# Kernel optimization log

Hardware: AMD Instinct MI355X
Metric: run time of the kernel (lower is better)

The kernel has to match this reference:

```python
import jax, jax.numpy as jnp
import numpy as np

TAU = 0.07
MIN_PIXELS = 3
LAMBDA_CF = 0.5
NUM_INST = 16  # labels in patch_mask are 0 (bg) .. NUM_INST
N, D = 65536, 256


def _l2norm(x, axis=-1):
    n = jnp.linalg.norm(x, axis=axis, keepdims=True)
    return x / jnp.maximum(n, 1e-12)


def setup_inputs() -> dict:
    key = jax.random.key(0)
    k1, k2, k3 = jax.random.split(key, 3)
    dp = jax.random.normal(k1, (N, D), dtype=jnp.float32)
    f_cf = jax.random.normal(k2, (N, D), dtype=jnp.float32)
    patch_mask = jax.random.randint(k3, (N,), 0, NUM_INST + 1, dtype=jnp.int32)
    return {"dp": dp, "f_cf": f_cf, "patch_mask": patch_mask}


def reference(dp, f_cf, patch_mask):
    K1 = NUM_INST + 1  # segment 0 = background, 1..K = instances
    labels = patch_mask
    dpn = _l2norm(dp)       # [N, D]
    cfn = _l2norm(f_cf)     # [N, D]

    ones = jnp.ones((labels.shape[0],), dtype=dp.dtype)
    cnt = jax.ops.segment_sum(ones, labels, num_segments=K1)         # [K1]
    sum_dp = jax.ops.segment_sum(dpn, labels, num_segments=K1)       # [K1, D]
    sum_cf = jax.ops.segment_sum(cfn, labels, num_segments=K1)       # [K1, D]
    safe_cnt = jnp.maximum(cnt, 1.0)

    mu_dp = _l2norm(sum_dp / safe_cnt[:, None])   # per-segment normalized mean of dp
    mu_cf = _l2norm(sum_cf / safe_cnt[:, None])   # per-segment normalized mean of f_cf
    mu_bg_dp = mu_dp[0]                           # [D]
    mu_bg_cf = mu_cf[0]                           # [D]

    # per-pixel similarities
    pos_t = jnp.sum(dpn * mu_dp[labels], axis=-1)      # dp . mu_{k(label)}
    neg_t = dpn @ mu_bg_dp                             # dp . mu_bg
    # -log(exp(p/tau)/(exp(p/tau)+exp(n/tau))) == softplus((n-p)/tau)
    pix_loss_t = jax.nn.softplus((neg_t - pos_t) / TAU)

    pos_cf = cfn @ mu_bg_cf                            # f_cf . mu_bg_cf (the 'pos' in the cf term)
    oth_cf = jnp.sum(cfn * mu_cf[labels], axis=-1)     # f_cf . mu_k_cf
    pix_loss_cf = jax.nn.softplus((oth_cf - pos_cf) / TAU)

    seg_loss_t = jax.ops.segment_sum(pix_loss_t, labels, num_segments=K1) / safe_cnt
    seg_loss_cf = jax.ops.segment_sum(pix_loss_cf, labels, num_segments=K1) / safe_cnt

    inst_ids = jnp.arange(K1)
    valid = (inst_ids > 0) & (cnt >= MIN_PIXELS)       # instances with enough pixels
    n_valid = jnp.maximum(jnp.sum(valid.astype(dp.dtype)), 1.0)

    loss_t = jnp.sum(jnp.where(valid, seg_loss_t, 0.0)) / n_valid
    loss_cf = jnp.sum(jnp.where(valid, seg_loss_cf, 0.0)) / n_valid
    return loss_t + LAMBDA_CF * loss_cf
```

## Files before the change

kernel.cpp:

```cpp
#include <hip/hip_runtime.h>
#include <math.h>

#define K1 17
#define SEG_F (K1 * 256)
#define PART_F (2 * SEG_F + 32)
#define NGRP 8
#define NPART 256

#define SCALE_SUM 65536.0f
#define INV_SUM   (1.0f / 65536.0f)
#define SCALE_L   8192.0f
#define INV_L     (1.0f / 8192.0f)
#define FP8_SCALE 16.0f
#define TAU_INV   (1.0f / 0.07f)

#define GRED_BASE 0
#define MU_BASE   (NGRP * 2 * SEG_F)
#define GCNT_OFF  (MU_BASE + 2 * SEG_F)
#define LT_OFF    (GCNT_OFF + K1)
#define LC_OFF    (LT_OFF + K1)
#define PART_BASE 78400
#define FP8D_BASE (PART_BASE + NPART * PART_F)

typedef float v2f __attribute__((ext_vector_type(2)));

template <int CTRL, int RMASK>
__device__ __forceinline__ float dpp_add(float x) {
    int t = __builtin_amdgcn_update_dpp(0, __float_as_int(x), CTRL, RMASK, 0xf, false);
    return x + __int_as_float(t);
}
__device__ __forceinline__ float wave_sum_nb(float x) {
    x = dpp_add<0x111, 0xf>(x);
    x = dpp_add<0x112, 0xf>(x);
    x = dpp_add<0x114, 0xf>(x);
    x = dpp_add<0x118, 0xf>(x);
    x = dpp_add<0x142, 0xa>(x);
    x = dpp_add<0x143, 0xc>(x);
    return x;
}
__device__ __forceinline__ float wave_sum(float x) {
    return __int_as_float(__builtin_amdgcn_readlane(__float_as_int(wave_sum_nb(x)), 63));
}
__device__ __forceinline__ float dot4s(const float4 v) {
    return v.x * v.x + v.y * v.y + v.z * v.z + v.w * v.w;
}
__device__ __forceinline__ float softplus_f(float x) {
    const float a = -fabsf(x) * 1.4426950408889634f;
    float e; asm("v_exp_f32 %0, %1" : "=v"(e) : "v"(a));
    float l; asm("v_log_f32 %0, %1" : "=v"(l) : "v"(1.0f + e));
    return fmaxf(x, 0.0f) + l * 0.6931471805599453f;
}
__device__ __forceinline__ float rsq_f(float x) {
    float r; asm("v_rsq_f32 %0, %1" : "=v"(r) : "v"(x));
    return r;
}

template <bool W8>
__device__ __forceinline__ void kA_commit(int* __restrict__ s, const float4 v, const float4 w,
                                          float nd, float nc, int l, int lane,
                                          uint2* __restrict__ q8)
{
    const float ir = rsq_f(fmaxf(nd, 1e-24f));
    const float jr = rsq_f(fmaxf(nc, 1e-24f));
    const float f = SCALE_SUM * ir;
    const float g = SCALE_SUM * jr;
    int* a = s + l * 256 + lane;
    atomicAdd(a,       (int)(v.x * f));
    atomicAdd(a + 64,  (int)(v.y * f));
    atomicAdd(a + 128, (int)(v.z * f));
    atomicAdd(a + 192, (int)(v.w * f));
    int* b = a + SEG_F;
    atomicAdd(b,       (int)(w.x * g));
    atomicAdd(b + 64,  (int)(w.y * g));
    atomicAdd(b + 128, (int)(w.z * g));
    atomicAdd(b + 192, (int)(w.w * g));
    if (W8) {
        const float fe = FP8_SCALE * ir;
        const float ge = FP8_SCALE * jr;
        int pd = __builtin_amdgcn_cvt_pk_fp8_f32(v.x * fe, v.y * fe, 0, false);
        pd     = __builtin_amdgcn_cvt_pk_fp8_f32(v.z * fe, v.w * fe, pd, true);
        int pc = __builtin_amdgcn_cvt_pk_fp8_f32(w.x * ge, w.y * ge, 0, false);
        pc     = __builtin_amdgcn_cvt_pk_fp8_f32(w.z * ge, w.w * ge, pc, true);
        *q8 = make_uint2((unsigned)pd, (unsigned)pc);
    }
}

template <bool W8>
__global__ __launch_bounds__(1024) void kA(const float4* __restrict__ dp, const float4* __restrict__ cf,
                                           const int* __restrict__ mask, float* __restrict__ part,
                                           uint2* __restrict__ q, int nPart, int nRows)
{
    __shared__ int s[2 * SEG_F];
    __shared__ int hist[K1];
    const int tid = threadIdx.x;
    for (int i = tid; i < 2 * SEG_F; i += 1024) s[i] = 0;
    if (tid < K1) hist[tid] = 0;
    __syncthreads();

    const int lane = tid & 63;
    const int wid = tid >> 6;
    const int rpb = (nRows + nPart - 1) / nPart;
    const int base = blockIdx.x * rpb;
    const int end = (base + rpb < nRows) ? base + rpb : nRows;

    int r = base + wid;
    for (; r + 16 < end; r += 32) {
        const int l0 = mask[r], l1 = mask[r + 16];
        const float4 v0 = dp[(size_t)r * 64 + lane];
        const float4 w0 = cf[(size_t)r * 64 + lane];
        const float4 v1 = dp[(size_t)(r + 16) * 64 + lane];
        const float4 w1 = cf[(size_t)(r + 16) * 64 + lane];
        const float nd0 = wave_sum(dot4s(v0));
        const float nc0 = wave_sum(dot4s(w0));
        const float nd1 = wave_sum(dot4s(v1));
        const float nc1 = wave_sum(dot4s(w1));
        kA_commit<W8>(s, v0, w0, nd0, nc0, l0, lane, q + (size_t)r * 64 + lane);
        kA_commit<W8>(s, v1, w1, nd1, nc1, l1, lane, q + (size_t)(r + 16) * 64 + lane);
        if (lane == 0) { atomicAdd(&hist[l0], 1); atomicAdd(&hist[l1], 1); }
    }
    for (; r < end; r += 16) {
        const int l0 = mask[r];
        const float4 v0 = dp[(size_t)r * 64 + lane];
        const float4 w0 = cf[(size_t)r * 64 + lane];
        const float nd0 = wave_sum(dot4s(v0));
        const float nc0 = wave_sum(dot4s(w0));
        kA_commit<W8>(s, v0, w0, nd0, nc0, l0, lane, q + (size_t)r * 64 + lane);
        if (lane == 0) atomicAdd(&hist[l0], 1);
    }
    __syncthreads();
    float* outp = part + (size_t)blockIdx.x * PART_F;
    for (int i = tid; i < 2 * SEG_F; i += 1024) outp[i] = (float)s[i] * INV_SUM;
    if (tid < K1) outp[2 * SEG_F + tid] = (float)hist[tid];
}

__global__ __launch_bounds__(256) void kRed(const float* __restrict__ part, float* __restrict__ gred, int nPart)
{
    const int col = blockIdx.x * 256 + threadIdx.x;
    const int g = blockIdx.y;
    const int per = nPart / NGRP;
    const float* p = part + (size_t)g * per * PART_F + col;
    float acc = 0.0f;
    for (int b = 0; b < per; ++b) acc += p[(size_t)b * PART_F];
    gred[g * (2 * SEG_F) + col] = acc;
}

__global__ __launch_bounds__(256) void k_mu(float* __restrict__ ws, int nPart)
{
    const int k = blockIdx.x, t = threadIdx.x;
    if (k == 0 && t < 2 * K1) ((int*)ws)[LT_OFF + t] = 0;
    __shared__ float C[256];
    float c = 0.0f;
    for (int b = t; b < nPart; b += 256) c += ws[PART_BASE + (size_t)b * PART_F + 2 * SEG_F + k];
    C[t] = c; __syncthreads();
    for (int s2 = 128; s2 > 0; s2 >>= 1) { if (t < s2) C[t] += C[t + s2]; __syncthreads(); }
    const float cnt = C[0];
    __syncthreads();
    float c0 = 0.0f;
    for (int b = t; b < nPart; b += 256) c0 += ws[PART_BASE + (size_t)b * PART_F + 2 * SEG_F];
    C[t] = c0; __syncthreads();
    for (int s2 = 128; s2 > 0; s2 >>= 1) { if (t < s2) C[t] += C[t + s2]; __syncthreads(); }
    const float cnt0 = C[0];

    const float safek = fmaxf(cnt, 1.0f), safe0 = fmaxf(cnt0, 1.0f);
    float sdk = 0, sck = 0, sd0 = 0, sc0 = 0;
    #pragma unroll
    for (int g = 0; g < NGRP; ++g) {
        const float* gr = ws + GRED_BASE + g * 2 * SEG_F;
        sdk += gr[k * 256 + t];  sck += gr[SEG_F + k * 256 + t];
        sd0 += gr[t];            sc0 += gr[SEG_F + t];
    }
    const float mdk = sdk / safek, mck = sck / safek;
    const float md0 = sd0 / safe0, mc0 = sc0 / safe0;
    __shared__ float A[256], B[256];
    A[t] = mdk * mdk; B[t] = mck * mck;
    __syncthreads();
    for (int s2 = 128; s2 > 0; s2 >>= 1) { if (t < s2) { A[t] += A[t + s2]; B[t] += B[t + s2]; } __syncthreads(); }
    const float idk = 1.0f / fmaxf(sqrtf(A[0]), 1e-12f);
    const float ick = 1.0f / fmaxf(sqrtf(B[0]), 1e-12f);
    __syncthreads();
    A[t] = md0 * md0; B[t] = mc0 * mc0;
    __syncthreads();
    for (int s2 = 128; s2 > 0; s2 >>= 1) { if (t < s2) { A[t] += A[t + s2]; B[t] += B[t + s2]; } __syncthreads(); }
    const float id0 = 1.0f / fmaxf(sqrtf(A[0]), 1e-12f);
    const float ic0 = 1.0f / fmaxf(sqrtf(B[0]), 1e-12f);
    const int dnat = 4 * (t & 63) + (t >> 6);
    ws[MU_BASE + k * 256 + dnat]         = md0 * id0 - mdk * idk;
    ws[MU_BASE + SEG_F + k * 256 + dnat] = mck * ick - mc0 * ic0;
    if (t == 0) ws[GCNT_OFF + k] = cnt;
}

__device__ __forceinline__ void q_commit(float dd, float dc, int l, int isl63,
                                         int* __restrict__ lt, int* __restrict__ lc)
{
    const float xt = dd * (TAU_INV / FP8_SCALE);
    const float xc = dc * (TAU_INV / FP8_SCALE);
    const float plt = softplus_f(xt);
    const float plc = softplus_f(xc);
    if (isl63) {
        atomicAdd(&lt[l], (int)(plt * SCALE_L + 0.5f));
        atomicAdd(&lc[l], (int)(plc * SCALE_L + 0.5f));
    }
}
__global__ __launch_bounds__(512) void k_loss8(const uint2* __restrict__ q,
                                               const int* __restrict__ mask, float* __restrict__ ws,
                                               int nBlocks, int nRows)
{
    __shared__ float4 dmud[SEG_F / 4], dmuc[SEG_F / 4];
    __shared__ int lt[K1], lc[K1];
    const int tid = threadIdx.x;
    const float4* musrc = (const float4*)(ws + MU_BASE);
    for (int i = tid; i < SEG_F / 4; i += 512) { dmud[i] = musrc[i]; dmuc[i] = musrc[SEG_F / 4 + i]; }
    if (tid < K1) { lt[tid] = 0; lc[tid] = 0; }
    __syncthreads();

    const int lane = tid & 63;
    const int wid = tid >> 6;
    const int rpb = (nRows + nBlocks - 1) / nBlocks;
    const int base = blockIdx.x * rpb;
    const int end = (base + rpb < nRows) ? base + rpb : nRows;
    const int isl63 = (lane == 63);

    int r = base + wid;
    for (; r + 8 < end; r += 16) {
        const int l0 = mask[r], l1 = mask[r + 8];
        const uint2 q0 = q[(size_t)r * 64 + lane];
        const uint2 q1 = q[(size_t)(r + 8) * 64 + lane];
        const float4 D0 = dmud[l0 * 64 + lane], C0 = dmuc[l0 * 64 + lane];
        const float4 D1 = dmud[l1 * 64 + lane], C1 = dmuc[l1 * 64 + lane];
        const v2f al0 = __builtin_amdgcn_cvt_pk_f32_fp8((int)q0.x, false), ah0 = __builtin_amdgcn_cvt_pk_f32_fp8((int)q0.x, true);
        const v2f bl0 = __builtin_amdgcn_cvt_pk_f32_fp8((int)q0.y, false), bh0 = __builtin_amdgcn_cvt_pk_f32_fp8((int)q0.y, true);
        const v2f al1 = __builtin_amdgcn_cvt_pk_f32_fp8((int)q1.x, false), ah1 = __builtin_amdgcn_cvt_pk_f32_fp8((int)q1.x, true);
        const v2f bl1 = __builtin_amdgcn_cvt_pk_f32_fp8((int)q1.y, false), bh1 = __builtin_amdgcn_cvt_pk_f32_fp8((int)q1.y, true);
        float dd0 = al0.x * D0.x + al0.y * D0.y + ah0.x * D0.z + ah0.y * D0.w;
        float dc0 = bl0.x * C0.x + bl0.y * C0.y + bh0.x * C0.z + bh0.y * C0.w;
        float dd1 = al1.x * D1.x + al1.y * D1.y + ah1.x * D1.z + ah1.y * D1.w;
        float dc1 = bl1.x * C1.x + bl1.y * C1.y + bh1.x * C1.z + bh1.y * C1.w;
        dd0 = wave_sum_nb(dd0); dc0 = wave_sum_nb(dc0);
        dd1 = wave_sum_nb(dd1); dc1 = wave_sum_nb(dc1);
        q_commit(dd0, dc0, l0, isl63, lt, lc);
        q_commit(dd1, dc1, l1, isl63, lt, lc);
    }
    for (; r < end; r += 8) {
        const int l0 = mask[r];
        const uint2 q0 = q[(size_t)r * 64 + lane];
        const float4 D0 = dmud[l0 * 64 + lane], C0 = dmuc[l0 * 64 + lane];
        const v2f al0 = __builtin_amdgcn_cvt_pk_f32_fp8((int)q0.x, false), ah0 = __builtin_amdgcn_cvt_pk_f32_fp8((int)q0.x, true);
        const v2f bl0 = __builtin_amdgcn_cvt_pk_f32_fp8((int)q0.y, false), bh0 = __builtin_amdgcn_cvt_pk_f32_fp8((int)q0.y, true);
        float dd0 = al0.x * D0.x + al0.y * D0.y + ah0.x * D0.z + ah0.y * D0.w;
        float dc0 = bl0.x * C0.x + bl0.y * C0.y + bh0.x * C0.z + bh0.y * C0.w;
        dd0 = wave_sum_nb(dd0); dc0 = wave_sum_nb(dc0);
        q_commit(dd0, dc0, l0, isl63, lt, lc);
    }
    __syncthreads();
    if (tid < K1) {
        atomicAdd((int*)ws + LT_OFF + tid, lt[tid]);
        atomicAdd((int*)ws + LC_OFF + tid, lc[tid]);
    }
}

__global__ __launch_bounds__(512) void k_lossraw(const float4* __restrict__ dp, const float4* __restrict__ cf,
                                                 const int* __restrict__ mask, float* __restrict__ ws,
                                                 int nBlocks, int nRows)
{
    __shared__ float4 dmud[SEG_F / 4], dmuc[SEG_F / 4];
    __shared__ int lt[K1], lc[K1];
    const int tid = threadIdx.x;
    const float4* musrc = (const float4*)(ws + MU_BASE);
    for (int i = tid; i < SEG_F / 4; i += 512) { dmud[i] = musrc[i]; dmuc[i] = musrc[SEG_F / 4 + i]; }
    if (tid < K1) { lt[tid] = 0; lc[tid] = 0; }
    __syncthreads();

    const int lane = tid & 63;
    const int wid = tid >> 6;
    const int rpb = (nRows + nBlocks - 1) / nBlocks;
    const int base = blockIdx.x * rpb;
    const int end = (base + rpb < nRows) ? base + rpb : nRows;
    const int isl63 = (lane == 63);

    for (int r = base + wid; r < end; r += 8) {
        const int l0 = mask[r];
        const float4 v0 = dp[(size_t)r * 64 + lane];
        const float4 w0 = cf[(size_t)r * 64 + lane];
        const float4 D0 = dmud[l0 * 64 + lane], C0 = dmuc[l0 * 64 + lane];
        float nd = dot4s(v0), nc = dot4s(w0);
        float dd = v0.x * D0.x + v0.y * D0.y + v0.z * D0.z + v0.w * D0.w;
        float dc = w0.x * C0.x + w0.y * C0.y + w0.z * C0.z + w0.w * C0.w;
        nd = wave_sum_nb(nd); nc = wave_sum_nb(nc);
        dd = wave_sum_nb(dd); dc = wave_sum_nb(dc);
        const float xt = dd * rsq_f(fmaxf(nd, 1e-24f)) * TAU_INV;
        const float xc = dc * rsq_f(fmaxf(nc, 1e-24f)) * TAU_INV;
        const float plt = softplus_f(xt);
        const float plc = softplus_f(xc);
        if (isl63) {
            atomicAdd(&lt[l0], (int)(plt * SCALE_L + 0.5f));
            atomicAdd(&lc[l0], (int)(plc * SCALE_L + 0.5f));
        }
    }
    __syncthreads();
    if (tid < K1) {
        atomicAdd((int*)ws + LT_OFF + tid, lt[tid]);
        atomicAdd((int*)ws + LC_OFF + tid, lc[tid]);
    }
}

__global__ void k_final(const float* __restrict__ ws, float* __restrict__ out)
{
    const int t = threadIdx.x;
    const int* LT = (const int*)ws + LT_OFF;
    const int* LC = (const int*)ws + LC_OFF;
    float vt = 0.0f, vc = 0.0f, nv = 0.0f;
    if (t >= 1 && t < K1) {
        const float cnt = ws[GCNT_OFF + t];
        if (cnt >= 3.0f) {
            const float safe = fmaxf(cnt, 1.0f);
            vt = (float)LT[t] * INV_L / safe;
            vc = (float)LC[t] * INV_L / safe;
            nv = 1.0f;
        }
    }
    #pragma unroll
    for (int o = 32; o > 0; o >>= 1) {
        vt += __shfl_xor(vt, o, 64);
        vc += __shfl_xor(vc, o, 64);
        nv += __shfl_xor(nv, o, 64);
    }
    if (t == 0) {
        const float n = fmaxf(nv, 1.0f);
        out[0] = vt / n + 0.5f * (vc / n);
    }
}

extern "C" void kernel_launch(void* const* d_in, const int* in_sizes, int n_in,
                              void* d_out, int out_size, void* d_ws, size_t ws_size,
                              hipStream_t stream)
{
    const float4* dp = (const float4*)d_in[0];
    const float4* cf = (const float4*)d_in[1];
    const int* mask  = (const int*)d_in[2];
    float* ws  = (float*)d_ws;
    float* out = (float*)d_out;
    const int nRows = in_sizes[2];

    uint2* q = (uint2*)((unsigned*)ws + FP8D_BASE);
    const bool use8 = (ws_size / 4) >= (size_t)FP8D_BASE + 2 * (size_t)nRows * 64;

    if (use8)
        kA<true><<<NPART, 1024, 0, stream>>>(dp, cf, mask, ws + PART_BASE, q, NPART, nRows);
    else
        kA<false><<<NPART, 1024, 0, stream>>>(dp, cf, mask, ws + PART_BASE, q, NPART, nRows);
    kRed<<<dim3(34, NGRP), 256, 0, stream>>>(ws + PART_BASE, ws + GRED_BASE, NPART);
    k_mu<<<K1, 256, 0, stream>>>(ws, NPART);
    const int nB3 = 1024;
    if (use8)
        k_loss8<<<nB3, 512, 0, stream>>>(q, mask, ws, nB3, nRows);
    else
        k_lossraw<<<nB3, 512, 0, stream>>>(dp, cf, mask, ws, nB3, nRows);
    k_final<<<1, 64, 0, stream>>>(ws, out);
}
```

Baseline: 80.60 us.

## Unroll kA to four rows per wave and fold final reduction into loss kernel

The first kernel now loads four dp/cf row pairs per wave per iteration instead of two, with asm keep-alive hints so the loads are issued together before the reductions. This raises memory-level parallelism in the bandwidth-bound normalisation pass at the cost of more registers. Separately, the standalone k_final launch is removed. Its work moves into a last-block-done epilogue of the loss kernel, driven by an atomic counter that k_mu zeroes, which saves one kernel launch and its gap.

Result: no change. 81.64 us (+1.3%).

```diff
diff --git a/kernel.cpp b/kernel.cpp
--- a/kernel.cpp
+++ b/kernel.cpp
@@ -19,10 +19,13 @@
 #define GCNT_OFF  (MU_BASE + 2 * SEG_F)
 #define LT_OFF    (GCNT_OFF + K1)
 #define LC_OFF    (LT_OFF + K1)
+#define DONE_OFF  (LC_OFF + K1)
 #define PART_BASE 78400
 #define FP8D_BASE (PART_BASE + NPART * PART_F)
 
 typedef float v2f __attribute__((ext_vector_type(2)));
+
+#define KEEP4(v) asm volatile("" :: "v"((v).x), "v"((v).y), "v"((v).z), "v"((v).w))
 
 template <int CTRL, int RMASK>
 __device__ __forceinline__ float dpp_add(float x) {
@@ -104,19 +107,30 @@
     const int end = (base + rpb < nRows) ? base + rpb : nRows;
 
     int r = base + wid;
-    for (; r + 16 < end; r += 32) {
-        const int l0 = mask[r], l1 = mask[r + 16];
-        const float4 v0 = dp[(size_t)r * 64 + lane];
-        const float4 w0 = cf[(size_t)r * 64 + lane];
-        const float4 v1 = dp[(size_t)(r + 16) * 64 + lane];
-        const float4 w1 = cf[(size_t)(r + 16) * 64 + lane];
-        const float nd0 = wave_sum(dot4s(v0));
-        const float nc0 = wave_sum(dot4s(w0));
-        const float nd1 = wave_sum(dot4s(v1));
-        const float nc1 = wave_sum(dot4s(w1));
+    for (; r + 48 < end; r += 64) {
+        const int l0 = mask[r], l1 = mask[r + 16], l2 = mask[r + 32], l3 = mask[r + 48];
+        float4 v0 = dp[(size_t)r * 64 + lane],        w0 = cf[(size_t)r * 64 + lane];
+        float4 v1 = dp[(size_t)(r + 16) * 64 + lane], w1 = cf[(size_t)(r + 16) * 64 + lane];
+        float4 v2 = dp[(size_t)(r + 32) * 64 + lane], w2 = cf[(size_t)(r + 32) * 64 + lane];
+        float4 v3 = dp[(size_t)(r + 48) * 64 + lane], w3 = cf[(size_t)(r + 48) * 64 + lane];
+        KEEP4(v0); KEEP4(w0); KEEP4(v1); KEEP4(w1);
+        KEEP4(v2); KEEP4(w2); KEEP4(v3); KEEP4(w3);
+        float nd0 = dot4s(v0), nc0 = dot4s(w0);
+        float nd1 = dot4s(v1), nc1 = dot4s(w1);
+        float nd2 = dot4s(v2), nc2 = dot4s(w2);
+        float nd3 = dot4s(v3), nc3 = dot4s(w3);
+        nd0 = wave_sum(nd0); nc0 = wave_sum(nc0);
+        nd1 = wave_sum(nd1); nc1 = wave_sum(nc1);
+        nd2 = wave_sum(nd2); nc2 = wave_sum(nc2);
+        nd3 = wave_sum(nd3); nc3 = wave_sum(nc3);
         kA_commit<W8>(s, v0, w0, nd0, nc0, l0, lane, q + (size_t)r * 64 + lane);
         kA_commit<W8>(s, v1, w1, nd1, nc1, l1, lane, q + (size_t)(r + 16) * 64 + lane);
-        if (lane == 0) { atomicAdd(&hist[l0], 1); atomicAdd(&hist[l1], 1); }
+        kA_commit<W8>(s, v2, w2, nd2, nc2, l2, lane, q + (size_t)(r + 32) * 64 + lane);
+        kA_commit<W8>(s, v3, w3, nd3, nc3, l3, lane, q + (size_t)(r + 48) * 64 + lane);
+        if (lane == 0) {
+            atomicAdd(&hist[l0], 1); atomicAdd(&hist[l1], 1);
+            atomicAdd(&hist[l2], 1); atomicAdd(&hist[l3], 1);
+        }
     }
     for (; r < end; r += 16) {
         const int l0 = mask[r];
@@ -147,7 +161,7 @@
 __global__ __launch_bounds__(256) void k_mu(float* __restrict__ ws, int nPart)
 {
     const int k = blockIdx.x, t = threadIdx.x;
-    if (k == 0 && t < 2 * K1) ((int*)ws)[LT_OFF + t] = 0;
+    if (k == 0 && t < 2 * K1 + 1) ((int*)ws)[LT_OFF + t] = 0;
     __shared__ float C[256];
     float c = 0.0f;
     for (int b = t; b < nPart; b += 256) c += ws[PART_BASE + (size_t)b * PART_F + 2 * SEG_F + k];
@@ -189,6 +203,45 @@
     if (t == 0) ws[GCNT_OFF + k] = cnt;
 }
 
+__device__ __forceinline__ void loss_epilogue(float* __restrict__ ws, float* __restrict__ out,
+                                              int* __restrict__ lt, int* __restrict__ lc,
+                                              int tid, int nBlocks)
+{
+    __syncthreads();
+    int* LT = (int*)ws + LT_OFF;
+    int* LC = (int*)ws + LC_OFF;
+    if (tid < K1) {
+        atomicAdd(&LT[tid], lt[tid]);
+        atomicAdd(&LC[tid], lc[tid]);
+    }
+    __syncthreads();
+    __shared__ int amLast;
+    if (tid == 0) amLast = (atomicAdd((int*)ws + DONE_OFF, 1) == nBlocks - 1);
+    __syncthreads();
+    if (amLast && tid < 64) {
+        float vt = 0.0f, vc = 0.0f, nv = 0.0f;
+        if (tid >= 1 && tid < K1) {
+            const float cnt = ws[GCNT_OFF + tid];
+            if (cnt >= 3.0f) {
+                const float safe = fmaxf(cnt, 1.0f);
+                vt = (float)atomicAdd(&LT[tid], 0) * INV_L / safe;
+                vc = (float)atomicAdd(&LC[tid], 0) * INV_L / safe;
+                nv = 1.0f;
+            }
+        }
+        #pragma unroll
+        for (int o = 32; o > 0; o >>= 1) {
+            vt += __shfl_xor(vt, o, 64);
+            vc += __shfl_xor(vc, o, 64);
+            nv += __shfl_xor(nv, o, 64);
+        }
+        if (tid == 0) {
+            const float n = fmaxf(nv, 1.0f);
+            out[0] = vt / n + 0.5f * (vc / n);
+        }
+    }
+}
+
 __device__ __forceinline__ void q_commit(float dd, float dc, int l, int isl63,
                                          int* __restrict__ lt, int* __restrict__ lc)
 {
@@ -203,7 +256,7 @@
 }
 __global__ __launch_bounds__(512) void k_loss8(const uint2* __restrict__ q,
                                                const int* __restrict__ mask, float* __restrict__ ws,
-                                               int nBlocks, int nRows)
+                                               float* __restrict__ out, int nBlocks, int nRows)
 {
     __shared__ float4 dmud[SEG_F / 4], dmuc[SEG_F / 4];
     __shared__ int lt[K1], lc[K1];
@@ -251,16 +304,12 @@
         dd0 = wave_sum_nb(dd0); dc0 = wave_sum_nb(dc0);
         q_commit(dd0, dc0, l0, isl63, lt, lc);
     }
-    __syncthreads();
-    if (tid < K1) {
-        atomicAdd((int*)ws + LT_OFF + tid, lt[tid]);
-        atomicAdd((int*)ws + LC_OFF + tid, lc[tid]);
-    }
+    loss_epilogue(ws, out, lt, lc, tid, nBlocks);
 }
 
 __global__ __launch_bounds__(512) void k_lossraw(const float4* __restrict__ dp, const float4* __restrict__ cf,
                                                  const int* __restrict__ mask, float* __restrict__ ws,
-                                                 int nBlocks, int nRows)
+                                                 float* __restrict__ out, int nBlocks, int nRows)
 {
     __shared__ float4 dmud[SEG_F / 4], dmuc[SEG_F / 4];
     __shared__ int lt[K1], lc[K1];
@@ -296,38 +345,7 @@
             atomicAdd(&lc[l0], (int)(plc * SCALE_L + 0.5f));
         }
     }
-    __syncthreads();
-    if (tid < K1) {
-        atomicAdd((int*)ws + LT_OFF + tid, lt[tid]);
-        atomicAdd((int*)ws + LC_OFF + tid, lc[tid]);
-    }
-}
-
-__global__ void k_final(const float* __restrict__ ws, float* __restrict__ out)
-{
-    const int t = threadIdx.x;
-    const int* LT = (const int*)ws + LT_OFF;
-    const int* LC = (const int*)ws + LC_OFF;
-    float vt = 0.0f, vc = 0.0f, nv = 0.0f;
-    if (t >= 1 && t < K1) {
-        const float cnt = ws[GCNT_OFF + t];
-        if (cnt >= 3.0f) {
-            const float safe = fmaxf(cnt, 1.0f);
-            vt = (float)LT[t] * INV_L / safe;
-            vc = (float)LC[t] * INV_L / safe;
-            nv = 1.0f;
-        }
-    }
-    #pragma unroll
-    for (int o = 32; o > 0; o >>= 1) {
-        vt += __shfl_xor(vt, o, 64);
-        vc += __shfl_xor(vc, o, 64);
-        nv += __shfl_xor(nv, o, 64);
-    }
-    if (t == 0) {
-        const float n = fmaxf(nv, 1.0f);
-        out[0] = vt / n + 0.5f * (vc / n);
-    }
+    loss_epilogue(ws, out, lt, lc, tid, nBlocks);
 }
 
 extern "C" void kernel_launch(void* const* d_in, const int* in_sizes, int n_in,
@@ -352,8 +370,7 @@
     k_mu<<<K1, 256, 0, stream>>>(ws, NPART);
     const int nB3 = 1024;
     if (use8)
-        k_loss8<<<nB3, 512, 0, stream>>>(q, mask, ws, nB3, nRows);
+        k_loss8<<<nB3, 512, 0, stream>>>(q, mask, ws, out, nB3, nRows);
     else
-        k_lossraw<<<nB3, 512, 0, stream>>>(dp, cf, mask, ws, nB3, nRows);
-    k_final<<<1, 64, 0, stream>>>(ws, out);
-}
+        k_lossraw<<<nB3, 512, 0, stream>>>(dp, cf, mask, ws, out, nB3, nRows);
+}
```
